# Kernel tuning notes

Measured on AMD Instinct MI355X. Metric: run time of the kernel, lower is better.

The kernel has to match this reference:

```python
import jax, jax.numpy as jnp
import numpy as np

B, C, N = 16, 512, 2048
MAXH, MAXW = 70, 40   # max_height, max_width with f_size=1
GY, GX = 80, 48       # virtual coordinate grid for input generation
BIG = 1_000_000


def setup_inputs() -> dict:
    key = jax.random.key(0)
    kf, kp, kv = jax.random.split(key, 3)
    features = jax.random.normal(kf, (B, C, N), dtype=jnp.float32)
    cells = jax.vmap(lambda k: jax.random.permutation(k, GY * GX)[:N])(
        jax.random.split(kp, B))
    ys = (cells // GX).astype(jnp.int32)
    xs = (cells % GX).astype(jnp.int32)
    valid = jax.random.bernoulli(kv, 0.9, (B, N)).at[:, 0].set(True)
    ys = jnp.where(valid, ys, -1)
    xs = jnp.where(valid, xs, -1)
    backend_feature = jnp.zeros((C, 1, 1), dtype=jnp.float32)  # dummy='zero'
    return {"features": features, "backend_feature": backend_feature,
            "ys": ys, "xs": xs}


def _one_sample(f, y, x, backend):
    # f: [C, N], y/x: [N] int, backend: [C, 1, 1]
    valid = y > -1
    min_y = jnp.min(jnp.where(valid, y, BIG))
    max_y = jnp.max(jnp.where(valid, y, -BIG))
    min_x = jnp.min(jnp.where(valid, x, BIG))
    max_x = jnp.max(jnp.where(valid, x, -BIG))
    h = max_y - min_y + 1
    w = max_x - min_x + 1
    # transpose if width > height
    trans = w > h
    yy = jnp.where(trans, x - min_x, y - min_y)
    xx = jnp.where(trans, y - min_y, x - min_x)
    H2 = jnp.where(trans, w, h)
    W2 = jnp.where(trans, h, w)
    # validation-mode centered crop/pad -> a single shift per axis
    hd = H2 - MAXH
    wd = W2 - MAXW
    sy = jnp.where(hd > 0, -((hd + 1) // 2), (1 - hd) // 2)
    sx = jnp.where(wd > 0, -((wd + 1) // 2), (1 - wd) // 2)
    oy = jnp.where(valid, yy + sy, -BIG)  # force drop for invalid points
    ox = jnp.where(valid, xx + sx, -BIG)
    canvas = jnp.zeros((C, MAXH, MAXW), f.dtype).at[:, oy, ox].set(f, mode='drop')
    mask = jnp.zeros((MAXH, MAXW), bool).at[oy, ox].set(True, mode='drop')
    # blend: real pixels from canvas, dummy backend elsewhere
    return jnp.where(mask[None], canvas, backend)


def reference(features, backend_feature, ys, xs):
    return jax.vmap(_one_sample, in_axes=(0, 0, 0, None))(
        features, ys, xs, backend_feature)
```

## Files before the change

kernel.cpp:

```cpp
#include <hip/hip_runtime.h>

#define BB 16
#define CC 512
#define NN 2048
#define MAXH 70
#define MAXW 40
#define NPIX (MAXH * MAXW)
#define BIGC 1000000

typedef float  f32x4 __attribute__((ext_vector_type(4)));
typedef int    i32x4 __attribute__((ext_vector_type(4)));

__global__ __launch_bounds__(256) void build_map_kernel(
    const int* __restrict__ ys, const int* __restrict__ xs,
    int* __restrict__ srcmap)
{
    const int b = blockIdx.x;
    const int tid = threadIdx.x;
    const int* __restrict__ y = ys + b * NN;
    const int* __restrict__ x = xs + b * NN;

    __shared__ int smap[NPIX];
    __shared__ int s0[256], s1[256], s2[256], s3[256];

    for (int p = tid; p < NPIX; p += 256) smap[p] = -1;

    int mny = BIGC, mxy = -BIGC, mnx = BIGC, mxx = -BIGC;
    for (int n = tid; n < NN; n += 256) {
        int yy = y[n];
        if (yy > -1) {
            int xx = x[n];
            mny = min(mny, yy); mxy = max(mxy, yy);
            mnx = min(mnx, xx); mxx = max(mxx, xx);
        }
    }
    s0[tid] = mny; s1[tid] = mxy; s2[tid] = mnx; s3[tid] = mxx;
    __syncthreads();
    for (int s = 128; s > 0; s >>= 1) {
        if (tid < s) {
            s0[tid] = min(s0[tid], s0[tid + s]);
            s1[tid] = max(s1[tid], s1[tid + s]);
            s2[tid] = min(s2[tid], s2[tid + s]);
            s3[tid] = max(s3[tid], s3[tid + s]);
        }
        __syncthreads();
    }
    const int min_y = s0[0], max_y = s1[0], min_x = s2[0], max_x = s3[0];
    const int h = max_y - min_y + 1;
    const int w = max_x - min_x + 1;
    const int trans = (w > h) ? 1 : 0;
    const int H2 = trans ? w : h;
    const int W2 = trans ? h : w;
    const int hd = H2 - MAXH;
    const int wd = W2 - MAXW;
    const int sy = (hd > 0) ? -((hd + 1) / 2) : ((1 - hd) / 2);
    const int sx = (wd > 0) ? -((wd + 1) / 2) : ((1 - wd) / 2);

    for (int n = tid; n < NN; n += 256) {
        int yy0 = y[n];
        if (yy0 <= -1) continue;
        int ry = yy0 - min_y;
        int rx = x[n] - min_x;
        int oy = (trans ? rx : ry) + sy;
        int ox = (trans ? ry : rx) + sx;
        if (oy < 0) oy += MAXH;
        if (ox < 0) ox += MAXW;
        if (oy >= 0 && oy < MAXH && ox >= 0 && ox < MAXW)
            atomicMax(&smap[oy * MAXW + ox], n);
    }
    __syncthreads();

    int* __restrict__ g = srcmap + b * NPIX;
    for (int p = tid; p < NPIX; p += 256) g[p] = smap[p];
}

__global__ __launch_bounds__(256) void fill_out_kernel(
    const float* __restrict__ feat, const float* __restrict__ backend,
    const int* __restrict__ srcmap, float* __restrict__ out)
{
    const int plane = blockIdx.x;
    const int b = plane >> 9;
    const int c = plane & (CC - 1);
    const float bv = backend[c];
    const float* __restrict__ frow = feat + (size_t)plane * NN;
    const i32x4* __restrict__ smap4 = (const i32x4*)(srcmap + b * NPIX);
    f32x4* __restrict__ orow4 = (f32x4*)(out + (size_t)plane * NPIX);

    for (int p4 = threadIdx.x; p4 < NPIX / 4; p4 += 256) {
        i32x4 s = smap4[p4];
        f32x4 v;
        v.x = (s.x >= 0) ? frow[s.x] : bv;
        v.y = (s.y >= 0) ? frow[s.y] : bv;
        v.z = (s.z >= 0) ? frow[s.z] : bv;
        v.w = (s.w >= 0) ? frow[s.w] : bv;
        __builtin_nontemporal_store(v, &orow4[p4]);
    }
}

__global__ __launch_bounds__(256) void fused_map_kernel(
    const float* __restrict__ feat, const float* __restrict__ backend,
    const int* __restrict__ ys, const int* __restrict__ xs,
    float* __restrict__ out)
{
    const int plane = blockIdx.x;
    const int b = plane >> 9;
    const int c = plane & (CC - 1);
    const int tid = threadIdx.x;
    const int* __restrict__ y = ys + b * NN;
    const int* __restrict__ x = xs + b * NN;

    __shared__ int smap[NPIX];
    __shared__ int s0[256], s1[256], s2[256], s3[256];

    for (int p = tid; p < NPIX; p += 256) smap[p] = -1;

    int mny = BIGC, mxy = -BIGC, mnx = BIGC, mxx = -BIGC;
    for (int n = tid; n < NN; n += 256) {
        int yy = y[n];
        if (yy > -1) {
            int xx = x[n];
            mny = min(mny, yy); mxy = max(mxy, yy);
            mnx = min(mnx, xx); mxx = max(mxx, xx);
        }
    }
    s0[tid] = mny; s1[tid] = mxy; s2[tid] = mnx; s3[tid] = mxx;
    __syncthreads();
    for (int s = 128; s > 0; s >>= 1) {
        if (tid < s) {
            s0[tid] = min(s0[tid], s0[tid + s]);
            s1[tid] = max(s1[tid], s1[tid + s]);
            s2[tid] = min(s2[tid], s2[tid + s]);
            s3[tid] = max(s3[tid], s3[tid + s]);
        }
        __syncthreads();
    }
    const int min_y = s0[0], max_y = s1[0], min_x = s2[0], max_x = s3[0];
    const int h = max_y - min_y + 1;
    const int w = max_x - min_x + 1;
    const int trans = (w > h) ? 1 : 0;
    const int H2 = trans ? w : h;
    const int W2 = trans ? h : w;
    const int hd = H2 - MAXH;
    const int wd = W2 - MAXW;
    const int sy = (hd > 0) ? -((hd + 1) / 2) : ((1 - hd) / 2);
    const int sx = (wd > 0) ? -((wd + 1) / 2) : ((1 - wd) / 2);

    for (int n = tid; n < NN; n += 256) {
        int yy0 = y[n];
        if (yy0 <= -1) continue;
        int ry = yy0 - min_y;
        int rx = x[n] - min_x;
        int oy = (trans ? rx : ry) + sy;
        int ox = (trans ? ry : rx) + sx;
        if (oy < 0) oy += MAXH;
        if (ox < 0) ox += MAXW;
        if (oy >= 0 && oy < MAXH && ox >= 0 && ox < MAXW)
            atomicMax(&smap[oy * MAXW + ox], n);
    }
    __syncthreads();

    const float bv = backend[c];
    const float* __restrict__ frow = feat + (size_t)plane * NN;
    f32x4* __restrict__ orow4 = (f32x4*)(out + (size_t)plane * NPIX);

    for (int p4 = tid; p4 < NPIX / 4; p4 += 256) {
        const int base = p4 * 4;
        int a0 = smap[base + 0];
        int a1 = smap[base + 1];
        int a2 = smap[base + 2];
        int a3 = smap[base + 3];
        f32x4 v;
        v.x = (a0 >= 0) ? frow[a0] : bv;
        v.y = (a1 >= 0) ? frow[a1] : bv;
        v.z = (a2 >= 0) ? frow[a2] : bv;
        v.w = (a3 >= 0) ? frow[a3] : bv;
        orow4[p4] = v;
    }
}

extern "C" void kernel_launch(void* const* d_in, const int* in_sizes, int n_in,
                              void* d_out, int out_size, void* d_ws, size_t ws_size,
                              hipStream_t stream) {
    const float* feat    = (const float*)d_in[0];
    const float* backend = (const float*)d_in[1];
    const int*   ys      = (const int*)d_in[2];
    const int*   xs      = (const int*)d_in[3];
    float* out = (float*)d_out;

    const size_t need = (size_t)BB * NPIX * sizeof(int);
    if (ws_size >= need) {
        int* srcmap = (int*)d_ws;
        build_map_kernel<<<BB, 256, 0, stream>>>(ys, xs, srcmap);
        fill_out_kernel<<<BB * CC, 256, 0, stream>>>(feat, backend, srcmap, out);
    } else {
        fused_map_kernel<<<BB * CC, 256, 0, stream>>>(feat, backend, ys, xs, out);
    }
}
```

Before: 185.1 us.

## Stage feature rows in LDS and process four channels per block

The fill kernel now copies four channels' full feature rows into shared memory with coalesced vector loads, then gathers from LDS instead of doing scattered global loads. Each block handles four channels, so the source-map loads are shared across them. This trades random global gathers for a dense streaming read of all features (including points that end up unused) and 32KB of LDS per block, which may cut occupancy.

New measurement: 163.7 us. 1.13x faster.

```diff
diff --git a/kernel.cpp b/kernel.cpp
--- a/kernel.cpp
+++ b/kernel.cpp
@@ -7,6 +7,7 @@
 #define MAXW 40
 #define NPIX (MAXH * MAXW)
 #define BIGC 1000000
+#define G 4
 
 typedef float  f32x4 __attribute__((ext_vector_type(4)));
 typedef int    i32x4 __attribute__((ext_vector_type(4)));
@@ -74,26 +75,44 @@
     for (int p = tid; p < NPIX; p += 256) g[p] = smap[p];
 }
 
-__global__ __launch_bounds__(256) void fill_out_kernel(
+__global__ __launch_bounds__(256) void fill_out_lds_kernel(
     const float* __restrict__ feat, const float* __restrict__ backend,
     const int* __restrict__ srcmap, float* __restrict__ out)
 {
-    const int plane = blockIdx.x;
-    const int b = plane >> 9;
-    const int c = plane & (CC - 1);
-    const float bv = backend[c];
-    const float* __restrict__ frow = feat + (size_t)plane * NN;
+    const int grp = blockIdx.x;
+    const int gpb = CC / G;
+    const int b  = grp / gpb;
+    const int c0 = (grp - b * gpb) * G;
+    const int tid = threadIdx.x;
+
+    __shared__ float sfeat[G * NN];
+
+    const f32x4* __restrict__ fsrc = (const f32x4*)(feat + ((size_t)b * CC + c0) * NN);
+    f32x4* __restrict__ sdst = (f32x4*)sfeat;
+    #pragma unroll
+    for (int i = 0; i < G * NN / 4 / 256; ++i)
+        sdst[tid + i * 256] = fsrc[tid + i * 256];
+    __syncthreads();
+
+    float bv[G];
+    #pragma unroll
+    for (int g = 0; g < G; ++g) bv[g] = backend[c0 + g];
+
     const i32x4* __restrict__ smap4 = (const i32x4*)(srcmap + b * NPIX);
-    f32x4* __restrict__ orow4 = (f32x4*)(out + (size_t)plane * NPIX);
-
-    for (int p4 = threadIdx.x; p4 < NPIX / 4; p4 += 256) {
+    f32x4* __restrict__ obase = (f32x4*)(out + ((size_t)b * CC + c0) * NPIX);
+
+    for (int p4 = tid; p4 < NPIX / 4; p4 += 256) {
         i32x4 s = smap4[p4];
-        f32x4 v;
-        v.x = (s.x >= 0) ? frow[s.x] : bv;
-        v.y = (s.y >= 0) ? frow[s.y] : bv;
-        v.z = (s.z >= 0) ? frow[s.z] : bv;
-        v.w = (s.w >= 0) ? frow[s.w] : bv;
-        __builtin_nontemporal_store(v, &orow4[p4]);
+        #pragma unroll
+        for (int g = 0; g < G; ++g) {
+            const float* sf = sfeat + g * NN;
+            f32x4 v;
+            v.x = (s.x >= 0) ? sf[s.x] : bv[g];
+            v.y = (s.y >= 0) ? sf[s.y] : bv[g];
+            v.z = (s.z >= 0) ? sf[s.z] : bv[g];
+            v.w = (s.w >= 0) ? sf[s.w] : bv[g];
+            __builtin_nontemporal_store(v, obase + (size_t)g * (NPIX / 4) + p4);
+        }
     }
 }
 
@@ -191,7 +210,7 @@
     if (ws_size >= need) {
         int* srcmap = (int*)d_ws;
         build_map_kernel<<<BB, 256, 0, stream>>>(ys, xs, srcmap);
-        fill_out_kernel<<<BB * CC, 256, 0, stream>>>(feat, backend, srcmap, out);
+        fill_out_lds_kernel<<<BB * CC / G, 256, 0, stream>>>(feat, backend, srcmap, out);
     } else {
         fused_map_kernel<<<BB * CC, 256, 0, stream>>>(feat, backend, ys, xs, out);
     }
```
